# Kernel optimization log

Hardware: AMD Instinct MI355X
Metric: run time of the kernel (lower is better)

Reference implementation:

```python
import jax, jax.numpy as jnp
import numpy as np

D_MODEL = 1024
N_HEADS = 16
HEAD_DIM = D_MODEL // N_HEADS


def setup_inputs() -> dict:
    key = jax.random.key(0)
    ks = jax.random.split(key, 12)
    B, L = 2, 2048
    s = 1.0 / np.sqrt(D_MODEL)
    inp = {
        "q": jax.random.normal(ks[0], (B, L, D_MODEL), dtype=jnp.float32),
        "k": jax.random.normal(ks[1], (B, L, D_MODEL), dtype=jnp.float32),
        "v": jax.random.normal(ks[2], (B, L, D_MODEL), dtype=jnp.float32),
        "mask": jax.random.randint(ks[3], (B, L), 0, 2).astype(jnp.bool_),
        "Wq": jax.random.normal(ks[4], (D_MODEL, D_MODEL), dtype=jnp.float32) * s,
        "bq": jnp.zeros((D_MODEL,), dtype=jnp.float32),
        "Wk": jax.random.normal(ks[5], (D_MODEL, D_MODEL), dtype=jnp.float32) * s,
        "bk": jnp.zeros((D_MODEL,), dtype=jnp.float32),
        "Wv": jax.random.normal(ks[6], (D_MODEL, D_MODEL), dtype=jnp.float32) * s,
        "bv": jnp.zeros((D_MODEL,), dtype=jnp.float32),
        "Wo": jax.random.normal(ks[7], (D_MODEL, D_MODEL), dtype=jnp.float32) * s,
        "bo": jnp.zeros((D_MODEL,), dtype=jnp.float32),
    }
    return inp


def reference(q, k, v, mask, Wq, bq, Wk, bk, Wv, bv, Wo, bo):
    B, Lq, _ = q.shape
    Lk = k.shape[1]
    # torch Linear: y = x @ W.T + b; W is [out, in]
    Q = (jnp.einsum("bld,ed->ble", q, Wq) + bq).reshape(B, Lq, N_HEADS, HEAD_DIM).transpose(0, 2, 1, 3)
    K = (jnp.einsum("bld,ed->ble", k, Wk) + bk).reshape(B, Lk, N_HEADS, HEAD_DIM).transpose(0, 2, 1, 3)
    V = (jnp.einsum("bld,ed->ble", v, Wv) + bv).reshape(B, Lk, N_HEADS, HEAD_DIM).transpose(0, 2, 1, 3)
    scale = 1.0 / np.sqrt(HEAD_DIM).astype(np.float32)
    scores = jnp.einsum("bhqd,bhkd->bhqk", Q, K) * scale  # [B,H,Lq,Lk]
    # mask: True = masked out; broadcast (B,1,1,Lk)
    scores = jnp.where(mask[:, None, None, :], -jnp.inf, scores)
    attn = jax.nn.softmax(scores, axis=-1)
    out = jnp.einsum("bhqk,bhkd->bhqd", attn, V)  # [B,H,Lq,hd]
    out = out.transpose(0, 2, 1, 3).reshape(B, Lq, D_MODEL)
    return jnp.einsum("bld,ed->ble", out, Wo) + bo
```

## Files before the change

kernel.cpp:

```cpp
#include <hip/hip_runtime.h>

typedef unsigned short u16;
typedef __bf16 bf16x8 __attribute__((ext_vector_type(8)));
typedef float f32x4 __attribute__((ext_vector_type(4)));
typedef unsigned int u32x4 __attribute__((ext_vector_type(4)));
typedef unsigned int u32x2 __attribute__((ext_vector_type(2)));

#define MFMA16(a, b, c) __builtin_amdgcn_mfma_f32_16x16x32_bf16((a), (b), (c), 0, 0, 0)

__device__ __forceinline__ u16 f2bf(float f) {
    unsigned u = __builtin_bit_cast(unsigned, f);
    u = u + 0x7FFFu + ((u >> 16) & 1u);
    return (u16)(u >> 16);
}
__device__ __forceinline__ unsigned pk2(float a, float b) {
    return (unsigned)f2bf(a) | ((unsigned)f2bf(b) << 16);
}
__device__ __forceinline__ u32x4 pk8(f32x4 a, f32x4 b) {
    u32x4 r;
    r[0] = pk2(a[0], a[1]); r[1] = pk2(a[2], a[3]);
    r[2] = pk2(b[0], b[1]); r[3] = pk2(b[2], b[3]);
    return r;
}
__device__ __forceinline__ unsigned cvtpk(float a, float b) {
    unsigned r;
    asm("v_cvt_pk_bf16_f32 %0, %1, %2" : "=v"(r) : "v"(a), "v"(b));
    return r;
}
__device__ __forceinline__ float exp2_fast(float x) {
    float r;
    asm("v_exp_f32 %0, %1" : "=v"(r) : "v"(x));
    return r;
}
__device__ __forceinline__ void lds_load16(const u16* g, u16* l) {
    __builtin_amdgcn_global_load_lds(
        (const __attribute__((address_space(1))) void*)g,
        (__attribute__((address_space(3))) void*)l, 16, 0, 0);
}

#define QSCALE 0.18033688011112042f
#define FIXMAX 13.0f

__global__ __launch_bounds__(256) void convert_bf16(
    const float* __restrict__ q, const float* __restrict__ k, const float* __restrict__ v,
    const float* __restrict__ Wq, const float* __restrict__ Wk, const float* __restrict__ Wv,
    const float* __restrict__ Wo, u16* __restrict__ dst)
{
    const size_t i = ((size_t)blockIdx.x * 256 + threadIdx.x) * 8;
    const size_t QE = 4194304, WE = 1048576;
    const float* s;
    if (i < QE) s = q + i;
    else if (i < 2 * QE) s = k + (i - QE);
    else if (i < 3 * QE) s = v + (i - 2 * QE);
    else {
        size_t j = i - 3 * QE;
        if (j < WE) s = Wq + j;
        else if (j < 2 * WE) s = Wk + (j - WE);
        else if (j < 3 * WE) s = Wv + (j - 2 * WE);
        else s = Wo + (j - 3 * WE);
    }
    f32x4 a = *(const f32x4*)s;
    f32x4 b = *(const f32x4*)(s + 4);
    *(u32x4*)(dst + i) = pk8(a, b);
}

__device__ __forceinline__ void gemm128_core(
    const u16* __restrict__ A, const u16* __restrict__ B,
    int m0, int n0, u16* As, u16* Bs, int tid, f32x4 acc[4][4])
{
    const int wv = tid >> 6, lane = tid & 63, quad = lane >> 4, l16 = lane & 15;
    const int mh = (wv >> 1) * 64, nh = (wv & 1) * 64;
    const int segA0 = wv * 128 + lane;
    const int segA1 = wv * 128 + 64 + lane;
    const int ra0 = segA0 >> 2, ca0 = (segA0 & 3) * 8;
    const int ra1 = segA1 >> 2, ca1 = (segA1 & 3) * 8;
    u16* ldsA0 = &As[(wv * 128) * 8];
    u16* ldsA1 = &As[(wv * 128 + 64) * 8];
    u16* ldsB0 = &Bs[(wv * 128) * 8];
    u16* ldsB1 = &Bs[(wv * 128 + 64) * 8];
    const u16* gA = A + (size_t)m0 * 1024;
    const u16* gB = B + (size_t)n0 * 1024;

    for (int t = 0; t < 32; t++) {
        const int k0 = t * 32;
        __syncthreads();
        lds_load16(gA + (size_t)ra0 * 1024 + k0 + ca0, ldsA0);
        lds_load16(gA + (size_t)ra1 * 1024 + k0 + ca1, ldsA1);
        lds_load16(gB + (size_t)ra0 * 1024 + k0 + ca0, ldsB0);
        lds_load16(gB + (size_t)ra1 * 1024 + k0 + ca1, ldsB1);
        __syncthreads();
        bf16x8 af[4], bfr[4];
        #pragma unroll
        for (int mi = 0; mi < 4; mi++)
            af[mi] = *(const bf16x8*)&As[(mh + mi * 16 + l16) * 32 + quad * 8];
        #pragma unroll
        for (int ni = 0; ni < 4; ni++)
            bfr[ni] = *(const bf16x8*)&Bs[(nh + ni * 16 + l16) * 32 + quad * 8];
        #pragma unroll
        for (int mi = 0; mi < 4; mi++)
            #pragma unroll
            for (int ni = 0; ni < 4; ni++)
                acc[mi][ni] = MFMA16(af[mi], bfr[ni], acc[mi][ni]);
    }
}

__global__ __launch_bounds__(256) void qkv_bf(
    const u16* __restrict__ qb, const u16* __restrict__ kb, const u16* __restrict__ vb,
    const u16* __restrict__ wq, const u16* __restrict__ wk, const u16* __restrict__ wvv,
    const float* __restrict__ bq, const float* __restrict__ bk, const float* __restrict__ bv,
    u16* __restrict__ Qh, u16* __restrict__ Kh, u16* __restrict__ Vt)
{
    __shared__ alignas(16) u16 As[128 * 32];
    __shared__ alignas(16) u16 Bs[128 * 32];
    const int z = blockIdx.z;
    const u16* A = (z == 0) ? qb : (z == 1) ? kb : vb;
    const u16* B = (z == 0) ? wq : (z == 1) ? wk : wvv;
    const float* bias = (z == 0) ? bq : (z == 1) ? bk : bv;
    const int tid = threadIdx.x;
    const int id = blockIdx.x + (blockIdx.y << 3);
    const int xd = id >> 5;
    const int yd = ((id & 7) << 2) | ((id >> 3) & 3);
    const int m0 = yd * 128, n0 = xd * 128;
    const int wv = tid >> 6, lane = tid & 63, quad = lane >> 4, l16 = lane & 15;
    const int mh = (wv >> 1) * 64, nh = (wv & 1) * 64;

    f32x4 acc[4][4];
    #pragma unroll
    for (int i = 0; i < 4; i++)
        #pragma unroll
        for (int j = 0; j < 4; j++) acc[i][j] = (f32x4){0.f, 0.f, 0.f, 0.f};

    gemm128_core(A, B, m0, n0, As, Bs, tid, acc);

    const float scl = (z == 0) ? QSCALE : 1.0f;
    u16* outp = (z == 0) ? Qh : (z == 1) ? Kh : Vt;
    #pragma unroll
    for (int ni = 0; ni < 4; ni++) {
        const int n = n0 + nh + ni * 16 + l16;
        const float bval = bias[n];
        const int h = n >> 6, d = n & 63;
        #pragma unroll
        for (int mi = 0; mi < 4; mi++) {
            const int mbase = m0 + mh + mi * 16 + quad * 4;
            #pragma unroll
            for (int r = 0; r < 4; r++) {
                const int m = mbase + r;
                const int bb = m >> 11, l = m & 2047;
                const float val = (acc[mi][ni][r] + bval) * scl;
                size_t idx;
                if (z < 2) idx = (((size_t)(bb * 16 + h) * 2048 + l) << 6) + d;
                else       idx = (((size_t)(bb * 16 + h) * 64 + d) << 11) + l;
                outp[idx] = f2bf(val);
            }
        }
    }
}

__global__ __launch_bounds__(256) void out_bf(
    const u16* __restrict__ Ob, const u16* __restrict__ wo,
    const float* __restrict__ bo, float* __restrict__ out)
{
    __shared__ alignas(16) u16 As[128 * 32];
    __shared__ alignas(16) u16 Bs[128 * 32];
    const int tid = threadIdx.x;
    const int id = blockIdx.x + (blockIdx.y << 3);
    const int xd = id >> 5;
    const int yd = ((id & 7) << 2) | ((id >> 3) & 3);
    const int m0 = yd * 128, n0 = xd * 128;
    const int wv = tid >> 6, lane = tid & 63, quad = lane >> 4, l16 = lane & 15;
    const int mh = (wv >> 1) * 64, nh = (wv & 1) * 64;

    f32x4 acc[4][4];
    #pragma unroll
    for (int i = 0; i < 4; i++)
        #pragma unroll
        for (int j = 0; j < 4; j++) acc[i][j] = (f32x4){0.f, 0.f, 0.f, 0.f};

    gemm128_core(Ob, wo, m0, n0, As, Bs, tid, acc);

    #pragma unroll
    for (int ni = 0; ni < 4; ni++) {
        const int n = n0 + nh + ni * 16 + l16;
        const float bval = bo[n];
        #pragma unroll
        for (int mi = 0; mi < 4; mi++) {
            const int mbase = m0 + mh + mi * 16 + quad * 4;
            #pragma unroll
            for (int r = 0; r < 4; r++)
                out[(size_t)(mbase + r) * 1024 + n] = acc[mi][ni][r] + bval;
        }
    }
}

__global__ __launch_bounds__(256) void attn6(
    const u16* __restrict__ Qh, const u16* __restrict__ Kh,
    const u16* __restrict__ Vt, const int* __restrict__ mask,
    u16* __restrict__ Ob)
{
    __shared__ alignas(16) u16 Ks[2][64 * 72];
    __shared__ alignas(16) u16 Vs[2][64 * 72];
    __shared__ alignas(16) u16 Ps[4][16 * 72];
    __shared__ alignas(16) float Ms[2][64];

    const int tid = threadIdx.x;
    const int blk = blockIdx.x;
    const int bh = blk & 31, qt = blk >> 5;
    const int b = bh >> 4, h = bh & 15;
    const int wv = tid >> 6, lane = tid & 63, quad = lane >> 4, l16 = lane & 15;

    const int qbase = qt * 128 + wv * 32;
    const u16* Qb = Qh + ((size_t)bh * 2048 + qbase) * 64;
    bf16x8 qf[2][2];
    #pragma unroll
    for (int sub = 0; sub < 2; sub++)
        #pragma unroll
        for (int hf = 0; hf < 2; hf++)
            qf[sub][hf] = *(const bf16x8*)(Qb + (sub * 16 + l16) * 64 + hf * 32 + quad * 8);

    const u32x4 onebits = {0x3F803F80u, 0x3F803F80u, 0x3F803F80u, 0x3F803F80u};
    const bf16x8 onesf = __builtin_bit_cast(bf16x8, onebits);

    const u16* Kb = Kh + (size_t)bh * 2048 * 64;
    const u16* Vb = Vt + (size_t)bh * 64 * 2048;
    const int* mb = mask + b * 2048;

    const int s0 = tid, s1 = tid + 256;
    const int r0 = s0 >> 3, c0 = (s0 & 7) * 8;
    const int r1 = s1 >> 3, c1 = (s1 & 7) * 8;
    const int rp0 = ((r0 >> 2) & 3) * 16 + (r0 >> 4) * 4 + (r0 & 3);
    const int rp1 = ((r1 >> 2) & 3) * 16 + (r1 >> 4) * 4 + (r1 & 3);

    u32x4 rk0 = *(const u32x4*)(Kb + r0 * 64 + c0);
    u32x4 rk1 = *(const u32x4*)(Kb + r1 * 64 + c1);
    u32x4 rv0 = *(const u32x4*)(Vb + (size_t)r0 * 2048 + c0);
    u32x4 rv1 = *(const u32x4*)(Vb + (size_t)r1 * 2048 + c1);
    float rm = (tid < 64) ? (mb[tid] ? -1e30f : -FIXMAX) : 0.f;

    f32x4 o[2][4];
    #pragma unroll
    for (int sub = 0; sub < 2; sub++)
        #pragma unroll
        for (int db = 0; db < 4; db++) o[sub][db] = (f32x4){0.f, 0.f, 0.f, 0.f};
    f32x4 accL[2];
    accL[0] = (f32x4){0.f, 0.f, 0.f, 0.f};
    accL[1] = (f32x4){0.f, 0.f, 0.f, 0.f};

    for (int kc = 0; kc < 32; kc++) {
        const int bi = kc & 1;
        u16* KsB = Ks[bi];
        u16* VsB = Vs[bi];
        *(u32x4*)&KsB[rp0 * 72 + c0] = rk0;
        *(u32x4*)&KsB[rp1 * 72 + c1] = rk1;
        *(u32x4*)&VsB[r0 * 72 + c0] = rv0;
        *(u32x4*)&VsB[r1 * 72 + c1] = rv1;
        if (tid < 64) Ms[bi][tid] = rm;
        __syncthreads();

        if (kc < 31) {
            const int off = (kc + 1) * 64;
            rk0 = *(const u32x4*)(Kb + (size_t)(off + r0) * 64 + c0);
            rk1 = *(const u32x4*)(Kb + (size_t)(off + r1) * 64 + c1);
            rv0 = *(const u32x4*)(Vb + (size_t)r0 * 2048 + off + c0);
            rv1 = *(const u32x4*)(Vb + (size_t)r1 * 2048 + off + c1);
            rm = (tid < 64) ? (mb[off + tid] ? -1e30f : -FIXMAX) : 0.f;
        }

        f32x4 st[2][4];
        __builtin_amdgcn_s_setprio(1);
        #pragma unroll
        for (int nb = 0; nb < 4; nb++) {
            const bf16x8 kf0 = *(const bf16x8*)&KsB[(nb * 16 + l16) * 72 + quad * 8];
            const bf16x8 kf1 = *(const bf16x8*)&KsB[(nb * 16 + l16) * 72 + 32 + quad * 8];
            #pragma unroll
            for (int sub = 0; sub < 2; sub++) {
                f32x4 z = (f32x4){0.f, 0.f, 0.f, 0.f};
                z = MFMA16(kf0, qf[sub][0], z);
                z = MFMA16(kf1, qf[sub][1], z);
                st[sub][nb] = z;
            }
        }
        __builtin_amdgcn_s_setprio(0);
        f32x4 mneg[4];
        #pragma unroll
        for (int nb = 0; nb < 4; nb++)
            mneg[nb] = *(const f32x4*)&Ms[bi][quad * 16 + nb * 4];

        bf16x8 pf[2][2];
        #pragma unroll
        for (int sub = 0; sub < 2; sub++) {
            #pragma unroll
            for (int nb = 0; nb < 4; nb++) {
                st[sub][nb] += mneg[nb];
                #pragma unroll
                for (int r = 0; r < 4; r++) st[sub][nb][r] = exp2_fast(st[sub][nb][r]);
            }

            u16* prow = &Ps[wv][l16 * 72];
            u32x4 w;
            w[0] = cvtpk(st[sub][0][0], st[sub][0][1]);
            w[1] = cvtpk(st[sub][0][2], st[sub][0][3]);
            w[2] = cvtpk(st[sub][1][0], st[sub][1][1]);
            w[3] = cvtpk(st[sub][1][2], st[sub][1][3]);
            *(u32x4*)&prow[quad * 16] = w;
            w[0] = cvtpk(st[sub][2][0], st[sub][2][1]);
            w[1] = cvtpk(st[sub][2][2], st[sub][2][3]);
            w[2] = cvtpk(st[sub][3][0], st[sub][3][1]);
            w[3] = cvtpk(st[sub][3][2], st[sub][3][3]);
            *(u32x4*)&prow[quad * 16 + 8] = w;

            asm volatile("s_waitcnt lgkmcnt(0)" ::: "memory");
            pf[sub][0] = *(const bf16x8*)&Ps[wv][l16 * 72 + quad * 8];
            pf[sub][1] = *(const bf16x8*)&Ps[wv][l16 * 72 + 32 + quad * 8];
            asm volatile("" ::: "memory");
        }

        __builtin_amdgcn_s_setprio(1);
        #pragma unroll
        for (int db = 0; db < 4; db++) {
            const bf16x8 vf0 = *(const bf16x8*)&VsB[(db * 16 + l16) * 72 + quad * 8];
            const bf16x8 vf1 = *(const bf16x8*)&VsB[(db * 16 + l16) * 72 + 32 + quad * 8];
            #pragma unroll
            for (int sub = 0; sub < 2; sub++) {
                o[sub][db] = MFMA16(pf[sub][0], vf0, o[sub][db]);
                o[sub][db] = MFMA16(pf[sub][1], vf1, o[sub][db]);
            }
        }
        #pragma unroll
        for (int sub = 0; sub < 2; sub++) {
            accL[sub] = MFMA16(pf[sub][0], onesf, accL[sub]);
            accL[sub] = MFMA16(pf[sub][1], onesf, accL[sub]);
        }
        __builtin_amdgcn_s_setprio(0);
        asm volatile("" ::: "memory");
    }

    #pragma unroll
    for (int sub = 0; sub < 2; sub++) {
        #pragma unroll
        for (int r = 0; r < 4; r++) {
            const float lr = __builtin_amdgcn_rcpf(accL[sub][r]);
            const int qrow = qt * 128 + wv * 32 + sub * 16 + quad * 4 + r;
            #pragma unroll
            for (int db = 0; db < 4; db++)
                Ob[((size_t)(b * 2048 + qrow)) * 1024 + h * 64 + db * 16 + l16] =
                    f2bf(o[sub][db][r] * lr);
        }
    }
}

__global__ __launch_bounds__(256) void qkv_gemm(
    const float* __restrict__ q, const float* __restrict__ k, const float* __restrict__ v,
    const float* __restrict__ Wq, const float* __restrict__ Wk, const float* __restrict__ Wv,
    const float* __restrict__ bq, const float* __restrict__ bk, const float* __restrict__ bv,
    u16* __restrict__ Qh, u16* __restrict__ Kh, u16* __restrict__ Vt)
{
    __shared__ alignas(16) u16 As[128 * 40];
    __shared__ alignas(16) u16 Bs[128 * 40];
    const int z = blockIdx.z;
    const float* A    = (z == 0) ? q  : (z == 1) ? k  : v;
    const float* W    = (z == 0) ? Wq : (z == 1) ? Wk : Wv;
    const float* bias = (z == 0) ? bq : (z == 1) ? bk : bv;
    const int tid = threadIdx.x;
    const int m0 = blockIdx.y * 128, n0 = blockIdx.x * 128;
    const int row = tid >> 1, cseg = tid & 1;
    const float* ga = A + (size_t)(m0 + row) * 1024 + cseg * 16;
    const float* gb = W + (size_t)(n0 + row) * 1024 + cseg * 16;
    const int wv = tid >> 6, lane = tid & 63, quad = lane >> 4, l16 = lane & 15;
    const int mh = (wv >> 1) * 64, nh = (wv & 1) * 64;

    f32x4 acc[4][4];
    for (int i = 0; i < 4; i++)
        for (int j = 0; j < 4; j++) acc[i][j] = (f32x4){0.f, 0.f, 0.f, 0.f};

    f32x4 ra[4], rb[4];
    for (int i = 0; i < 4; i++) {
        ra[i] = *(const f32x4*)(ga + i * 4);
        rb[i] = *(const f32x4*)(gb + i * 4);
    }
    for (int t = 0; t < 32; t++) {
        __syncthreads();
        *(u32x4*)&As[row * 40 + cseg * 16]     = pk8(ra[0], ra[1]);
        *(u32x4*)&As[row * 40 + cseg * 16 + 8] = pk8(ra[2], ra[3]);
        *(u32x4*)&Bs[row * 40 + cseg * 16]     = pk8(rb[0], rb[1]);
        *(u32x4*)&Bs[row * 40 + cseg * 16 + 8] = pk8(rb[2], rb[3]);
        __syncthreads();
        if (t < 31) {
            const int k0 = (t + 1) * 32;
            for (int i = 0; i < 4; i++) {
                ra[i] = *(const f32x4*)(ga + k0 + i * 4);
                rb[i] = *(const f32x4*)(gb + k0 + i * 4);
            }
        }
        bf16x8 af[4], bfr[4];
        for (int mi = 0; mi < 4; mi++)
            af[mi] = *(const bf16x8*)&As[(mh + mi * 16 + l16) * 40 + quad * 8];
        for (int ni = 0; ni < 4; ni++)
            bfr[ni] = *(const bf16x8*)&Bs[(nh + ni * 16 + l16) * 40 + quad * 8];
        for (int mi = 0; mi < 4; mi++)
            for (int ni = 0; ni < 4; ni++)
                acc[mi][ni] = MFMA16(af[mi], bfr[ni], acc[mi][ni]);
    }
    const float scl = (z == 0) ? QSCALE : 1.0f;
    u16* outp = (z == 0) ? Qh : (z == 1) ? Kh : Vt;
    for (int ni = 0; ni < 4; ni++) {
        const int n = n0 + nh + ni * 16 + l16;
        const float bval = bias[n];
        const int h = n >> 6, d = n & 63;
        for (int mi = 0; mi < 4; mi++) {
            const int mbase = m0 + mh + mi * 16 + quad * 4;
            for (int r = 0; r < 4; r++) {
                const int m = mbase + r;
                const int bb = m >> 11, l = m & 2047;
                const float val = (acc[mi][ni][r] + bval) * scl;
                size_t idx;
                if (z < 2) idx = (((size_t)(bb * 16 + h) * 2048 + l) << 6) + d;
                else       idx = (((size_t)(bb * 16 + h) * 64 + d) << 11) + l;
                outp[idx] = f2bf(val);
            }
        }
    }
}

__global__ __launch_bounds__(256) void out_gemm(
    const u16* __restrict__ Ob, const float* __restrict__ Wo,
    const float* __restrict__ bo, float* __restrict__ out)
{
    __shared__ alignas(16) u16 As[128 * 40];
    __shared__ alignas(16) u16 Bs[128 * 40];
    const int tid = threadIdx.x;
    const int m0 = blockIdx.y * 128, n0 = blockIdx.x * 128;
    const int row = tid >> 1, cseg = tid & 1;
    const u16* ga = Ob + (size_t)(m0 + row) * 1024 + cseg * 16;
    const float* gb = Wo + (size_t)(n0 + row) * 1024 + cseg * 16;
    const int wv = tid >> 6, lane = tid & 63, quad = lane >> 4, l16 = lane & 15;
    const int mh = (wv >> 1) * 64, nh = (wv & 1) * 64;

    f32x4 acc[4][4];
    for (int i = 0; i < 4; i++)
        for (int j = 0; j < 4; j++) acc[i][j] = (f32x4){0.f, 0.f, 0.f, 0.f};

    u32x4 ra0 = *(const u32x4*)(ga);
    u32x4 ra1 = *(const u32x4*)(ga + 8);
    f32x4 rb[4];
    for (int i = 0; i < 4; i++) rb[i] = *(const f32x4*)(gb + i * 4);

    for (int t = 0; t < 32; t++) {
        __syncthreads();
        *(u32x4*)&As[row * 40 + cseg * 16]     = ra0;
        *(u32x4*)&As[row * 40 + cseg * 16 + 8] = ra1;
        *(u32x4*)&Bs[row * 40 + cseg * 16]     = pk8(rb[0], rb[1]);
        *(u32x4*)&Bs[row * 40 + cseg * 16 + 8] = pk8(rb[2], rb[3]);
        __syncthreads();
        if (t < 31) {
            const int k0 = (t + 1) * 32;
            ra0 = *(const u32x4*)(ga + k0);
            ra1 = *(const u32x4*)(ga + k0 + 8);
            for (int i = 0; i < 4; i++) rb[i] = *(const f32x4*)(gb + k0 + i * 4);
        }
        bf16x8 af[4], bfr[4];
        for (int mi = 0; mi < 4; mi++)
            af[mi] = *(const bf16x8*)&As[(mh + mi * 16 + l16) * 40 + quad * 8];
        for (int ni = 0; ni < 4; ni++)
            bfr[ni] = *(const bf16x8*)&Bs[(nh + ni * 16 + l16) * 40 + quad * 8];
        for (int mi = 0; mi < 4; mi++)
            for (int ni = 0; ni < 4; ni++)
                acc[mi][ni] = MFMA16(af[mi], bfr[ni], acc[mi][ni]);
    }
    for (int ni = 0; ni < 4; ni++) {
        const int n = n0 + nh + ni * 16 + l16;
        const float bval = bo[n];
        for (int mi = 0; mi < 4; mi++) {
            const int mbase = m0 + mh + mi * 16 + quad * 4;
            for (int r = 0; r < 4; r++)
                out[(size_t)(mbase + r) * 1024 + n] = acc[mi][ni][r] + bval;
        }
    }
}

extern "C" void kernel_launch(void* const* d_in, const int* in_sizes, int n_in,
                              void* d_out, int out_size, void* d_ws, size_t ws_size,
                              hipStream_t stream)
{
    (void)in_sizes; (void)n_in; (void)out_size;
    const float* q  = (const float*)d_in[0];
    const float* k  = (const float*)d_in[1];
    const float* v  = (const float*)d_in[2];
    const int* mask = (const int*)d_in[3];
    const float* Wq = (const float*)d_in[4];
    const float* bq = (const float*)d_in[5];
    const float* Wk = (const float*)d_in[6];
    const float* bk = (const float*)d_in[7];
    const float* Wv = (const float*)d_in[8];
    const float* bv = (const float*)d_in[9];
    const float* Wo = (const float*)d_in[10];
    const float* bo = (const float*)d_in[11];
    float* out = (float*)d_out;

    u16* ws = (u16*)d_ws;
    const size_t QE = 4194304, WE = 1048576;
    const size_t NEED = (6 * QE + 4 * WE) * 2;

    if (ws_size >= NEED) {
        u16* qbf = ws;
        u16* kbf = ws + QE;
        u16* vbf = ws + 2 * QE;
        u16* wqb = ws + 3 * QE;
        u16* wkb = wqb + WE;
        u16* wvb = wqb + 2 * WE;
        u16* wob = wqb + 3 * WE;
        u16* Qh  = ws + 3 * QE + 4 * WE;
        u16* Kh  = Qh + QE;
        u16* Vth = Qh + 2 * QE;
        u16* Obp = qbf;
        convert_bf16<<<dim3(8192), 256, 0, stream>>>(q, k, v, Wq, Wk, Wv, Wo, ws);
        qkv_bf<<<dim3(8, 32, 3), 256, 0, stream>>>(qbf, kbf, vbf, wqb, wkb, wvb,
                                                   bq, bk, bv, Qh, Kh, Vth);
        attn6<<<dim3(512), 256, 0, stream>>>(Qh, Kh, Vth, mask, Obp);
        out_bf<<<dim3(8, 32), 256, 0, stream>>>(Obp, wob, bo, out);
    } else {
        u16* Qh  = ws;
        u16* Kh  = ws + QE;
        u16* Vth = ws + 2 * QE;
        u16* Obp = ws + 3 * QE;
        qkv_gemm<<<dim3(8, 32, 3), 256, 0, stream>>>(q, k, v, Wq, Wk, Wv,
                                                     bq, bk, bv, Qh, Kh, Vth);
        attn6<<<dim3(512), 256, 0, stream>>>(Qh, Kh, Vth, mask, Obp);
        out_gemm<<<dim3(8, 32), 256, 0, stream>>>(Obp, Wo, bo, out);
    }
}
```

Baseline: 229.3 us.

## Keep softmax probabilities in registers by permuting K/V tile row layout

Changes the row permutation used when staging K and V tiles into shared memory, so the MFMA score output layout lines up directly with the A-operand layout of the P·V MFMA. This removes the per-wave shared-memory round trip through the Ps buffer and its explicit waitcnt. The mask bias is also folded into the MFMA accumulator init instead of being added afterwards. Correctness depends on the new permutation matching the register layout exactly, including the Ms index mapping.

Measured after the change: 225.4 us. Within noise of the previous version (-1.7%).

```diff
diff --git a/kernel.cpp b/kernel.cpp
--- a/kernel.cpp
+++ b/kernel.cpp
@@ -192,14 +192,13 @@
     }
 }
 
-__global__ __launch_bounds__(256) void attn6(
+__global__ __launch_bounds__(256) void attn8(
     const u16* __restrict__ Qh, const u16* __restrict__ Kh,
     const u16* __restrict__ Vt, const int* __restrict__ mask,
     u16* __restrict__ Ob)
 {
     __shared__ alignas(16) u16 Ks[2][64 * 72];
     __shared__ alignas(16) u16 Vs[2][64 * 72];
-    __shared__ alignas(16) u16 Ps[4][16 * 72];
     __shared__ alignas(16) float Ms[2][64];
 
     const int tid = threadIdx.x;
@@ -227,8 +226,8 @@
     const int s0 = tid, s1 = tid + 256;
     const int r0 = s0 >> 3, c0 = (s0 & 7) * 8;
     const int r1 = s1 >> 3, c1 = (s1 & 7) * 8;
-    const int rp0 = ((r0 >> 2) & 3) * 16 + (r0 >> 4) * 4 + (r0 & 3);
-    const int rp1 = ((r1 >> 2) & 3) * 16 + (r1 >> 4) * 4 + (r1 & 3);
+    const int rp0 = (r0 & 3) | (((r0 >> 3) & 3) << 2) | (((r0 >> 2) & 1) << 4) | ((r0 >> 5) << 5);
+    const int rp1 = (r1 & 3) | (((r1 >> 3) & 3) << 2) | (((r1 >> 2) & 1) << 4) | ((r1 >> 5) << 5);
 
     u32x4 rk0 = *(const u32x4*)(Kb + r0 * 64 + c0);
     u32x4 rk1 = *(const u32x4*)(Kb + r1 * 64 + c1);
@@ -269,49 +268,37 @@
         __builtin_amdgcn_s_setprio(1);
         #pragma unroll
         for (int nb = 0; nb < 4; nb++) {
+            const f32x4 mneg = *(const f32x4*)&Ms[bi][((nb >> 1) << 5) + (quad << 3) + ((nb & 1) << 2)];
             const bf16x8 kf0 = *(const bf16x8*)&KsB[(nb * 16 + l16) * 72 + quad * 8];
             const bf16x8 kf1 = *(const bf16x8*)&KsB[(nb * 16 + l16) * 72 + 32 + quad * 8];
             #pragma unroll
             for (int sub = 0; sub < 2; sub++) {
-                f32x4 z = (f32x4){0.f, 0.f, 0.f, 0.f};
+                f32x4 z = mneg;
                 z = MFMA16(kf0, qf[sub][0], z);
                 z = MFMA16(kf1, qf[sub][1], z);
                 st[sub][nb] = z;
             }
         }
         __builtin_amdgcn_s_setprio(0);
-        f32x4 mneg[4];
-        #pragma unroll
-        for (int nb = 0; nb < 4; nb++)
-            mneg[nb] = *(const f32x4*)&Ms[bi][quad * 16 + nb * 4];
 
         bf16x8 pf[2][2];
         #pragma unroll
         for (int sub = 0; sub < 2; sub++) {
             #pragma unroll
-            for (int nb = 0; nb < 4; nb++) {
-                st[sub][nb] += mneg[nb];
+            for (int nb = 0; nb < 4; nb++)
                 #pragma unroll
                 for (int r = 0; r < 4; r++) st[sub][nb][r] = exp2_fast(st[sub][nb][r]);
-            }
-
-            u16* prow = &Ps[wv][l16 * 72];
-            u32x4 w;
-            w[0] = cvtpk(st[sub][0][0], st[sub][0][1]);
-            w[1] = cvtpk(st[sub][0][2], st[sub][0][3]);
-            w[2] = cvtpk(st[sub][1][0], st[sub][1][1]);
-            w[3] = cvtpk(st[sub][1][2], st[sub][1][3]);
-            *(u32x4*)&prow[quad * 16] = w;
-            w[0] = cvtpk(st[sub][2][0], st[sub][2][1]);
-            w[1] = cvtpk(st[sub][2][2], st[sub][2][3]);
-            w[2] = cvtpk(st[sub][3][0], st[sub][3][1]);
-            w[3] = cvtpk(st[sub][3][2], st[sub][3][3]);
-            *(u32x4*)&prow[quad * 16 + 8] = w;
-
-            asm volatile("s_waitcnt lgkmcnt(0)" ::: "memory");
-            pf[sub][0] = *(const bf16x8*)&Ps[wv][l16 * 72 + quad * 8];
-            pf[sub][1] = *(const bf16x8*)&Ps[wv][l16 * 72 + 32 + quad * 8];
-            asm volatile("" ::: "memory");
+            u32x4 w0, w1;
+            w0[0] = cvtpk(st[sub][0][0], st[sub][0][1]);
+            w0[1] = cvtpk(st[sub][0][2], st[sub][0][3]);
+            w0[2] = cvtpk(st[sub][1][0], st[sub][1][1]);
+            w0[3] = cvtpk(st[sub][1][2], st[sub][1][3]);
+            w1[0] = cvtpk(st[sub][2][0], st[sub][2][1]);
+            w1[1] = cvtpk(st[sub][2][2], st[sub][2][3]);
+            w1[2] = cvtpk(st[sub][3][0], st[sub][3][1]);
+            w1[3] = cvtpk(st[sub][3][2], st[sub][3][3]);
+            pf[sub][0] = __builtin_bit_cast(bf16x8, w0);
+            pf[sub][1] = __builtin_bit_cast(bf16x8, w1);
         }
 
         __builtin_amdgcn_s_setprio(1);
@@ -515,7 +502,7 @@
         convert_bf16<<<dim3(8192), 256, 0, stream>>>(q, k, v, Wq, Wk, Wv, Wo, ws);
         qkv_bf<<<dim3(8, 32, 3), 256, 0, stream>>>(qbf, kbf, vbf, wqb, wkb, wvb,
                                                    bq, bk, bv, Qh, Kh, Vth);
-        attn6<<<dim3(512), 256, 0, stream>>>(Qh, Kh, Vth, mask, Obp);
+        attn8<<<dim3(512), 256, 0, stream>>>(Qh, Kh, Vth, mask, Obp);
         out_bf<<<dim3(8, 32), 256, 0, stream>>>(Obp, wob, bo, out);
     } else {
         u16* Qh  = ws;
@@ -524,7 +511,7 @@
         u16* Obp = ws + 3 * QE;
         qkv_gemm<<<dim3(8, 32, 3), 256, 0, stream>>>(q, k, v, Wq, Wk, Wv,
                                                      bq, bk, bv, Qh, Kh, Vth);
-        attn6<<<dim3(512), 256, 0, stream>>>(Qh, Kh, Vth, mask, Obp);
+        attn8<<<dim3(512), 256, 0, stream>>>(Qh, Kh, Vth, mask, Obp);
         out_gemm<<<dim3(8, 32), 256, 0, stream>>>(Obp, Wo, bo, out);
     }
 }
```
